# Kernel optimization log

Measured on AMD Instinct MI355X. Metric: run time of the kernel, lower is better.

Reference implementation:

```python
import jax, jax.numpy as jnp
import numpy as np

T, D, FF, E, R = 4096, 1024, 2048, 4, 16
LORA_SCALE = 32.0 / 16.0  # alpha / r


def setup_inputs() -> dict:
    key = jax.random.key(0)
    ks = jax.random.split(key, 12)
    return {
        "x": jax.random.normal(ks[0], (T, D), jnp.float32),
        "gate_w": jax.random.normal(ks[1], (E, D), jnp.float32) * 0.03,
        "gate_up_w": jax.random.normal(ks[2], (D, 2 * FF), jnp.float32)[None].repeat(E, 0) * 0.0
                     + jax.random.normal(ks[2], (E, D, 2 * FF), jnp.float32) * 0.03,
        "gate_up_b": jax.random.normal(ks[3], (E, 2 * FF), jnp.float32) * 0.01,
        "down_w": jax.random.normal(ks[4], (E, FF, D), jnp.float32) * 0.02,
        "down_b": jax.random.normal(ks[5], (E, D), jnp.float32) * 0.01,
        "A_gate": jax.random.normal(ks[6], (E, R, D), jnp.float32) * 0.02,
        "B_gate": jax.random.normal(ks[7], (E, FF, R), jnp.float32) * 0.02,
        "A_up": jax.random.normal(ks[8], (E, R, D), jnp.float32) * 0.02,
        "B_up": jax.random.normal(ks[9], (E, FF, R), jnp.float32) * 0.02,
        "A_down": jax.random.normal(ks[10], (E, R, FF), jnp.float32) * 0.02,
        "B_down": jax.random.normal(ks[11], (E, D, R), jnp.float32) * 0.02,
        "top_k": 2,
    }


def reference(x, gate_w, gate_up_w, gate_up_b, down_w, down_b,
              A_gate, B_gate, A_up, B_up, A_down, B_down, top_k):
    t, d = x.shape
    e = gate_w.shape[0]
    # --- router: logits, softmax (fp32), top-k, renormalize ---
    router_logits = x @ gate_w.T                                   # [T,E]
    rw = jax.nn.softmax(router_logits.astype(jnp.float32), axis=1)
    top_w, sel = jax.lax.top_k(rw, top_k)                          # [T,k]
    top_w = top_w / jnp.sum(top_w, axis=-1, keepdims=True)
    top_w = top_w.astype(x.dtype)
    # dense per-token per-expert combine weights (scatter of top-k weights)
    w = jnp.zeros((t, e), x.dtype).at[jnp.arange(t)[:, None], sel].add(top_w)  # [T,E]
    # --- per-expert SwiGLU MLP with LoRA (vectorized over experts) ---
    gu = jnp.einsum('td,edf->etf', x, gate_up_w) + gate_up_b[:, None, :]       # [E,T,2FF]
    ff = gu.shape[-1] // 2
    gate = gu[..., :ff] + jnp.einsum('td,erd,efr->etf', x, A_gate, B_gate) * LORA_SCALE
    up = gu[..., ff:] + jnp.einsum('td,erd,efr->etf', x, A_up, B_up) * LORA_SCALE
    act = jax.nn.silu(gate) * up                                               # [E,T,FF]
    down = jnp.einsum('etf,efd->etd', act, down_w) + down_b[:, None, :]
    down = down + jnp.einsum('etf,erf,edr->etd', act, A_down, B_down) * LORA_SCALE
    # --- weighted scatter-combine ---
    final = jnp.einsum('etd,te->td', down, w)                                  # [T,D]
    return final, router_logits
```

## Files before the change

kernel.cpp:

```cpp
#include <hip/hip_runtime.h>

#define T_TOK 4096
#define DIM   1024
#define FFD   2048
#define NEXP  4
#define NRP   8704
#define MTILES 68

typedef unsigned short u16;
typedef __attribute__((ext_vector_type(8))) short short8;
typedef __attribute__((ext_vector_type(4))) float f32x4;
typedef __attribute__((ext_vector_type(8))) unsigned short u16x8;
typedef __attribute__((ext_vector_type(4))) unsigned short u16x4;

typedef __attribute__((address_space(1))) unsigned int as1_u32;
typedef __attribute__((address_space(3))) unsigned int as3_u32;

__device__ __forceinline__ u16 f2bf(float f) {
  union { float f; unsigned u; } v; v.f = f;
  unsigned u = v.u;
  return (u16)((u + 0x7fffu + ((u >> 16) & 1u)) >> 16);
}
__device__ __forceinline__ float bf2f(u16 h) {
  union { unsigned u; float f; } v; v.u = ((unsigned)h) << 16;
  return v.f;
}
__device__ __forceinline__ void gload16(const void* g, void* l) {
  __builtin_amdgcn_global_load_lds((const as1_u32*)g, (as3_u32*)l, 16, 0, 0);
}

__global__ void router_k(const float* __restrict__ x, const float* __restrict__ gw,
                         float* __restrict__ logits_out, int* __restrict__ sel,
                         float* __restrict__ selw) {
  int t = blockIdx.x;
  int lane = threadIdx.x;
  float xv[16];
#pragma unroll
  for (int i = 0; i < 16; ++i) xv[i] = x[(size_t)t * DIM + lane + i * 64];
  float l[4];
#pragma unroll
  for (int e = 0; e < 4; ++e) {
    float s = 0.f;
#pragma unroll
    for (int i = 0; i < 16; ++i) s += xv[i] * gw[e * DIM + lane + i * 64];
#pragma unroll
    for (int off = 32; off > 0; off >>= 1) s += __shfl_xor(s, off, 64);
    l[e] = s;
  }
  if (lane == 0) {
#pragma unroll
    for (int e = 0; e < 4; ++e) logits_out[(size_t)t * 4 + e] = l[e];
    int e0 = 0; float b0 = l[0];
    for (int e = 1; e < 4; ++e) if (l[e] > b0) { b0 = l[e]; e0 = e; }
    int e1 = -1; float b1 = -3.4e38f;
    for (int e = 0; e < 4; ++e) if (e != e0 && l[e] > b1) { b1 = l[e]; e1 = e; }
    float p1 = expf(b1 - b0);
    float w0 = 1.f / (1.f + p1);
    sel[2 * t] = e0; sel[2 * t + 1] = e1;
    selw[2 * t] = w0; selw[2 * t + 1] = 1.f - w0;
  }
}

__global__ void scan_k(const int* __restrict__ sel, int* __restrict__ pos,
                       int* __restrict__ offs, int* __restrict__ rowtok,
                       int* __restrict__ pairrow) {
  __shared__ int base[4];
  __shared__ int wsum[16];
  __shared__ int off_s[5];
  int tid = threadIdx.x, lane = tid & 63, wid = tid >> 6;
  if (tid < 4) base[tid] = 0;
  __syncthreads();
  for (int chunk = 0; chunk < 4; ++chunk) {
    int t = chunk * 1024 + tid;
    int e0 = sel[2 * t], e1 = sel[2 * t + 1];
    for (int e = 0; e < 4; ++e) {
      bool f = (e0 == e) || (e1 == e);
      unsigned long long m = __ballot(f);
      int within = __popcll(m & ((1ull << lane) - 1ull));
      if (lane == 0) wsum[wid] = __popcll(m);
      __syncthreads();
      int wbase = 0, tot = 0;
      for (int i = 0; i < 16; ++i) { int v = wsum[i]; if (i < wid) wbase += v; tot += v; }
      if (f) {
        int p = base[e] + wbase + within;
        if (e0 == e) pos[2 * t] = p; else pos[2 * t + 1] = p;
      }
      __syncthreads();
      if (tid == 0) base[e] += tot;
      __syncthreads();
    }
  }
  if (tid == 0) {
    int o = 0;
    for (int e = 0; e < 4; ++e) { off_s[e] = o; o += ((base[e] + 127) >> 7) << 7; }
    off_s[4] = o;
    for (int i = 0; i < 5; ++i) offs[i] = off_s[i];
  }
  __syncthreads();
  for (int r = tid; r < NRP; r += 1024) rowtok[r] = -1;
  __syncthreads();
  for (int t = tid; t < T_TOK; t += 1024) {
#pragma unroll
    for (int s = 0; s < 2; ++s) {
      int e = sel[2 * t + s];
      int rr = off_s[e] + pos[2 * t + s];
      pairrow[2 * t + s] = rr;
      rowtok[rr] = t;
    }
  }
}

__global__ void gather_k(const float* __restrict__ x, const int* __restrict__ rowtok,
                         u16* __restrict__ xg) {
  int r = blockIdx.x, tid = threadIdx.x;
  int t = rowtok[r];
  float4 v = make_float4(0.f, 0.f, 0.f, 0.f);
  if (t >= 0) v = ((const float4*)(x + (size_t)t * DIM))[tid];
  u16x4 o;
  o[0] = f2bf(v.x); o[1] = f2bf(v.y); o[2] = f2bf(v.z); o[3] = f2bf(v.w);
  ((u16x4*)(xg + (size_t)r * DIM))[tid] = o;
}

__global__ void cvtA_k(const float* __restrict__ Ag, const float* __restrict__ Au,
                       const float* __restrict__ Ad, u16* __restrict__ abgu,
                       u16* __restrict__ adb) {
  int g = blockIdx.x * 256 + threadIdx.x;
  if (g < 32768) {
    int flat = g * 4;
    int e = flat >> 15;
    int rem = flat & 32767;
    int q = rem >> 10;
    int d = rem & 1023;
    const float* src = (q < 16) ? (Ag + ((size_t)e * 16 + q) * DIM + d)
                                : (Au + ((size_t)e * 16 + (q - 16)) * DIM + d);
    float4 v = *(const float4*)src;
    u16x4 o; o[0] = f2bf(v.x); o[1] = f2bf(v.y); o[2] = f2bf(v.z); o[3] = f2bf(v.w);
    *(u16x4*)(abgu + (size_t)flat) = o;
  } else {
    int flat = (g - 32768) * 4;
    float4 v = *(const float4*)(Ad + flat);
    u16x4 o; o[0] = f2bf(v.x); o[1] = f2bf(v.y); o[2] = f2bf(v.z); o[3] = f2bf(v.w);
    *(u16x4*)(adb + (size_t)flat) = o;
  }
}

__global__ void xa_k(const u16* __restrict__ xg, const u16* __restrict__ abgu,
                     const int* __restrict__ offs, float* __restrict__ xagu) {
  int r0 = blockIdx.x * 2, lane = threadIdx.x;
  int e = 0;
  if (r0 >= offs[1]) e = 1;
  if (r0 >= offs[2]) e = 2;
  if (r0 >= offs[3]) e = 3;
  float x0[16], x1[16];
#pragma unroll
  for (int i = 0; i < 4; ++i) {
    u16x4 v0 = ((const u16x4*)(xg + (size_t)r0 * DIM))[lane + i * 64];
    u16x4 v1 = ((const u16x4*)(xg + (size_t)(r0 + 1) * DIM))[lane + i * 64];
#pragma unroll
    for (int j = 0; j < 4; ++j) { x0[i * 4 + j] = bf2f(v0[j]); x1[i * 4 + j] = bf2f(v1[j]); }
  }
  const u16* A = abgu + (size_t)e * 32 * DIM;
  for (int q = 0; q < 32; ++q) {
    float s0 = 0.f, s1 = 0.f;
#pragma unroll
    for (int i = 0; i < 4; ++i) {
      u16x4 av = ((const u16x4*)(A + (size_t)q * DIM))[lane + i * 64];
#pragma unroll
      for (int j = 0; j < 4; ++j) {
        float a = bf2f(av[j]);
        s0 += x0[i * 4 + j] * a; s1 += x1[i * 4 + j] * a;
      }
    }
#pragma unroll
    for (int off = 32; off > 0; off >>= 1) { s0 += __shfl_xor(s0, off, 64); s1 += __shfl_xor(s1, off, 64); }
    if (lane == 0) { xagu[(size_t)r0 * 32 + q] = s0; xagu[(size_t)(r0 + 1) * 32 + q] = s1; }
  }
}

__global__ void aad_k(const u16* __restrict__ act, const u16* __restrict__ adb,
                      const int* __restrict__ offs, float* __restrict__ aad) {
  int r0 = blockIdx.x * 2, lane = threadIdx.x;
  int e = 0;
  if (r0 >= offs[1]) e = 1;
  if (r0 >= offs[2]) e = 2;
  if (r0 >= offs[3]) e = 3;
  float x0[32], x1[32];
#pragma unroll
  for (int i = 0; i < 8; ++i) {
    u16x4 v0 = ((const u16x4*)(act + (size_t)r0 * FFD))[lane + i * 64];
    u16x4 v1 = ((const u16x4*)(act + (size_t)(r0 + 1) * FFD))[lane + i * 64];
#pragma unroll
    for (int j = 0; j < 4; ++j) { x0[i * 4 + j] = bf2f(v0[j]); x1[i * 4 + j] = bf2f(v1[j]); }
  }
  const u16* A = adb + (size_t)e * 16 * FFD;
  for (int q = 0; q < 16; ++q) {
    float s0 = 0.f, s1 = 0.f;
#pragma unroll
    for (int i = 0; i < 8; ++i) {
      u16x4 av = ((const u16x4*)(A + (size_t)q * FFD))[lane + i * 64];
#pragma unroll
      for (int j = 0; j < 4; ++j) {
        float a = bf2f(av[j]);
        s0 += x0[i * 4 + j] * a; s1 += x1[i * 4 + j] * a;
      }
    }
#pragma unroll
    for (int off = 32; off > 0; off >>= 1) { s0 += __shfl_xor(s0, off, 64); s1 += __shfl_xor(s1, off, 64); }
    if (lane == 0) { aad[(size_t)r0 * 16 + q] = s0; aad[(size_t)(r0 + 1) * 16 + q] = s1; }
  }
}

__global__ void transpose_k(const float* __restrict__ in, u16* __restrict__ out,
                            int K, int N) {
  int e = blockIdx.z;
  int n0 = blockIdx.x * 32, k0 = blockIdx.y * 32;
  const float* I = in + (size_t)e * K * N;
  u16* O = out + (size_t)e * N * K;
  __shared__ u16 tile[32][33];
#pragma unroll
  for (int i = 0; i < 4; ++i) {
    int k = k0 + threadIdx.y + i * 8;
    tile[threadIdx.y + i * 8][threadIdx.x] = f2bf(I[(size_t)k * N + n0 + threadIdx.x]);
  }
  __syncthreads();
#pragma unroll
  for (int i = 0; i < 4; ++i) {
    int n = n0 + threadIdx.y + i * 8;
    O[(size_t)n * K + k0 + threadIdx.x] = tile[threadIdx.x][threadIdx.y + i * 8];
  }
}

__global__ __launch_bounds__(256) void gemm1_k(
    const u16* __restrict__ xg, const u16* __restrict__ wgu_t,
    const float* __restrict__ gub, const float* __restrict__ Bg,
    const float* __restrict__ Bu, const float* __restrict__ xagu,
    const int* __restrict__ offs, u16* __restrict__ act) {
  __shared__ __align__(16) u16 sAB[8192];
  u16* sA = sAB;
  u16* sB = sAB + 4096;
  int tid = threadIdx.x, w = tid >> 6, lane = tid & 63;
  int orig = blockIdx.x;
  int wg = (orig & 7) * 272 + (orig >> 3);
  int f0 = (wg & 31) * 64;
  int row0 = (wg >> 5) * 128;
  int e = 0;
  if (row0 >= offs[1]) e = 1;
  if (row0 >= offs[2]) e = 2;
  if (row0 >= offs[3]) e = 3;

  int srow = w * 32 + (lane >> 2);
  int scol = ((lane & 3) ^ ((lane >> 3) & 3)) * 8;
  const u16* gA = xg + (size_t)(row0 + srow) * DIM + scol;
  int n1 = srow, n2 = srow + 16;
  int gr1 = (n1 < 64) ? (f0 + n1) : (2048 + f0 + n1 - 64);
  int gr2 = (n2 < 64) ? (f0 + n2) : (2048 + f0 + n2 - 64);
  const u16* gB1 = wgu_t + ((size_t)e << 22) + (size_t)gr1 * DIM + scol;
  const u16* gB2 = wgu_t + ((size_t)e << 22) + (size_t)gr2 * DIM + scol;
  u16* lA = sA + w * 1024;
  u16* lB = sB + w * 1024;
  int fo = (((lane >> 4) ^ ((lane >> 1) & 3))) * 8;

  f32x4 acc[2][8];
#pragma unroll
  for (int i = 0; i < 2; ++i)
#pragma unroll
    for (int j = 0; j < 8; ++j) acc[i][j] = f32x4{0.f, 0.f, 0.f, 0.f};

  for (int kk = 0; kk < DIM; kk += 32) {
    __syncthreads();
    gload16(gA + kk, lA);
    gload16(gA + 16 * DIM + kk, lA + 512);
    gload16(gB1 + kk, lB);
    gload16(gB2 + kk, lB + 512);
    __syncthreads();
    short8 a[2], b[8];
#pragma unroll
    for (int mi = 0; mi < 2; ++mi)
      a[mi] = *(const short8*)&sA[(w * 32 + mi * 16 + (lane & 15)) * 32 + fo];
#pragma unroll
    for (int ni = 0; ni < 8; ++ni)
      b[ni] = *(const short8*)&sB[(ni * 16 + (lane & 15)) * 32 + fo];
#pragma unroll
    for (int mi = 0; mi < 2; ++mi)
#pragma unroll
      for (int ni = 0; ni < 8; ++ni)
        acc[mi][ni] = __builtin_amdgcn_mfma_f32_16x16x32_bf16(a[mi], b[ni], acc[mi][ni], 0, 0, 0);
  }

  __syncthreads();
  {
    int r = tid >> 1, kh = tid & 1;
    int sw = (r >> 1) & 3;
    int o0 = r * 32 + ((2 * kh + 0) ^ sw) * 8;
    int o1 = r * 32 + ((2 * kh + 1) ^ sw) * 8;
    u16 tmp[16];
    if (kh == 0) {
#pragma unroll
      for (int q = 0; q < 16; ++q) tmp[q] = f2bf(2.f * xagu[(size_t)(row0 + r) * 32 + q]);
    } else {
#pragma unroll
      for (int q = 0; q < 16; ++q) tmp[q] = 0;
      tmp[0] = 0x3f80;
    }
    *(u16x8*)&sA[o0] = *(u16x8*)&tmp[0];
    *(u16x8*)&sA[o1] = *(u16x8*)&tmp[8];
    int f = (r < 64) ? (f0 + r) : (f0 + r - 64);
    const float* Bsrc = (r < 64) ? Bg : Bu;
    float bias = gub[e * 4096 + ((r < 64) ? f : (2048 + f))];
    if (kh == 0) {
#pragma unroll
      for (int q = 0; q < 16; ++q) tmp[q] = f2bf(Bsrc[((size_t)e * FFD + f) * 16 + q]);
    } else {
#pragma unroll
      for (int q = 0; q < 16; ++q) tmp[q] = 0;
      tmp[0] = f2bf(bias);
    }
    *(u16x8*)&sB[o0] = *(u16x8*)&tmp[0];
    *(u16x8*)&sB[o1] = *(u16x8*)&tmp[8];
  }
  __syncthreads();
  {
    short8 a[2], b[4];
#pragma unroll
    for (int mi = 0; mi < 2; ++mi)
      a[mi] = *(const short8*)&sA[(w * 32 + mi * 16 + (lane & 15)) * 32 + fo];
#pragma unroll
    for (int ni = 0; ni < 4; ++ni)
      b[ni] = *(const short8*)&sB[(ni * 16 + (lane & 15)) * 32 + fo];
#pragma unroll
    for (int mi = 0; mi < 2; ++mi)
#pragma unroll
      for (int ni = 0; ni < 4; ++ni)
        acc[mi][ni] = __builtin_amdgcn_mfma_f32_16x16x32_bf16(a[mi], b[ni], acc[mi][ni], 0, 0, 0);
  }
  __syncthreads();
  {
    int r = tid >> 1, kh = tid & 1;
    int sw = (r >> 1) & 3;
    int o0 = r * 32 + ((2 * kh + 0) ^ sw) * 8;
    int o1 = r * 32 + ((2 * kh + 1) ^ sw) * 8;
    u16 tmp[16];
    if (kh == 0) {
#pragma unroll
      for (int q = 0; q < 16; ++q) tmp[q] = f2bf(2.f * xagu[(size_t)(row0 + r) * 32 + 16 + q]);
    } else {
#pragma unroll
      for (int q = 0; q < 16; ++q) tmp[q] = 0;
      tmp[0] = 0x3f80;
    }
    *(u16x8*)&sA[o0] = *(u16x8*)&tmp[0];
    *(u16x8*)&sA[o1] = *(u16x8*)&tmp[8];
  }
  __syncthreads();
  {
    short8 a[2], b[4];
#pragma unroll
    for (int mi = 0; mi < 2; ++mi)
      a[mi] = *(const short8*)&sA[(w * 32 + mi * 16 + (lane & 15)) * 32 + fo];
#pragma unroll
    for (int ni = 0; ni < 4; ++ni)
      b[ni] = *(const short8*)&sB[((ni + 4) * 16 + (lane & 15)) * 32 + fo];
#pragma unroll
    for (int mi = 0; mi < 2; ++mi)
#pragma unroll
      for (int ni = 0; ni < 4; ++ni)
        acc[mi][ni + 4] = __builtin_amdgcn_mfma_f32_16x16x32_bf16(a[mi], b[ni], acc[mi][ni + 4], 0, 0, 0);
  }
  __syncthreads();
#pragma unroll
  for (int mi = 0; mi < 2; ++mi)
#pragma unroll
    for (int ni = 0; ni < 4; ++ni)
#pragma unroll
      for (int j = 0; j < 4; ++j) {
        int lr = w * 32 + mi * 16 + (lane >> 4) * 4 + j;
        int lc = ni * 16 + (lane & 15);
        float g = acc[mi][ni][j];
        float u = acc[mi][ni + 4][j];
        float s = g / (1.f + __expf(-g));
        sAB[lr * 64 + lc] = f2bf(s * u);
      }
  __syncthreads();
#pragma unroll
  for (int it = 0; it < 4; ++it) {
    int idx = it * 256 + tid;
    int rr = idx >> 3, c8 = (idx & 7) * 8;
    *(u16x8*)(act + (size_t)(row0 + rr) * FFD + f0 + c8) = *(const u16x8*)&sAB[rr * 64 + c8];
  }
}

__global__ __launch_bounds__(256) void gemm2_k(
    const u16* __restrict__ act, const u16* __restrict__ wd_t,
    const float* __restrict__ db, const float* __restrict__ Bd,
    const float* __restrict__ aad, const int* __restrict__ offs,
    u16* __restrict__ down) {
  __shared__ __align__(16) u16 sAB[8192];
  u16* sA = sAB;
  u16* sB = sAB + 4096;
  int tid = threadIdx.x, w = tid >> 6, lane = tid & 63;
  int orig = blockIdx.x;
  int wg = (orig & 7) * 68 + (orig >> 3);
  int n0 = (wg & 7) * 128;
  int row0 = (wg >> 3) * 128;
  int ks = blockIdx.y;
  size_t kbase = (size_t)ks * 1024;
  int e = 0;
  if (row0 >= offs[1]) e = 1;
  if (row0 >= offs[2]) e = 2;
  if (row0 >= offs[3]) e = 3;
  int wm = w >> 1, wn = w & 1;

  int srow = w * 32 + (lane >> 2);
  int scol = ((lane & 3) ^ ((lane >> 3) & 3)) * 8;
  const u16* gA = act + (size_t)(row0 + srow) * FFD + kbase + scol;
  const u16* gB = wd_t + (size_t)e * DIM * FFD + (size_t)(n0 + srow) * FFD + kbase + scol;
  u16* lA = sA + w * 1024;
  u16* lB = sB + w * 1024;
  int fo = (((lane >> 4) ^ ((lane >> 1) & 3))) * 8;

  f32x4 acc[4][4];
#pragma unroll
  for (int i = 0; i < 4; ++i)
#pragma unroll
    for (int j = 0; j < 4; ++j) acc[i][j] = f32x4{0.f, 0.f, 0.f, 0.f};

  for (int kk = 0; kk < 1024; kk += 32) {
    __syncthreads();
    gload16(gA + kk, lA);
    gload16(gA + 16 * FFD + kk, lA + 512);
    gload16(gB + kk, lB);
    gload16(gB + 16 * FFD + kk, lB + 512);
    __syncthreads();
    short8 a[4], b[4];
#pragma unroll
    for (int mi = 0; mi < 4; ++mi)
      a[mi] = *(const short8*)&sA[(wm * 64 + mi * 16 + (lane & 15)) * 32 + fo];
#pragma unroll
    for (int ni = 0; ni < 4; ++ni)
      b[ni] = *(const short8*)&sB[(wn * 64 + ni * 16 + (lane & 15)) * 32 + fo];
#pragma unroll
    for (int mi = 0; mi < 4; ++mi)
#pragma unroll
      for (int ni = 0; ni < 4; ++ni)
        acc[mi][ni] = __builtin_amdgcn_mfma_f32_16x16x32_bf16(a[mi], b[ni], acc[mi][ni], 0, 0, 0);
  }

  if (ks == 0) {
    __syncthreads();
    {
      int r = tid >> 1, kh = tid & 1;
      int sw = (r >> 1) & 3;
      int o0 = r * 32 + ((2 * kh + 0) ^ sw) * 8;
      int o1 = r * 32 + ((2 * kh + 1) ^ sw) * 8;
      u16 tmp[16];
      if (kh == 0) {
#pragma unroll
        for (int q = 0; q < 16; ++q) tmp[q] = f2bf(2.f * aad[(size_t)(row0 + r) * 16 + q]);
      } else {
#pragma unroll
        for (int q = 0; q < 16; ++q) tmp[q] = 0;
        tmp[0] = 0x3f80;
      }
      *(u16x8*)&sA[o0] = *(u16x8*)&tmp[0];
      *(u16x8*)&sA[o1] = *(u16x8*)&tmp[8];
      if (kh == 0) {
#pragma unroll
        for (int q = 0; q < 16; ++q) tmp[q] = f2bf(Bd[((size_t)e * DIM + n0 + r) * 16 + q]);
      } else {
#pragma unroll
        for (int q = 0; q < 16; ++q) tmp[q] = 0;
        tmp[0] = f2bf(db[e * DIM + n0 + r]);
      }
      *(u16x8*)&sB[o0] = *(u16x8*)&tmp[0];
      *(u16x8*)&sB[o1] = *(u16x8*)&tmp[8];
    }
    __syncthreads();
    {
      short8 a[4], b[4];
#pragma unroll
      for (int mi = 0; mi < 4; ++mi)
        a[mi] = *(const short8*)&sA[(wm * 64 + mi * 16 + (lane & 15)) * 32 + fo];
#pragma unroll
      for (int ni = 0; ni < 4; ++ni)
        b[ni] = *(const short8*)&sB[(wn * 64 + ni * 16 + (lane & 15)) * 32 + fo];
#pragma unroll
      for (int mi = 0; mi < 4; ++mi)
#pragma unroll
        for (int ni = 0; ni < 4; ++ni)
          acc[mi][ni] = __builtin_amdgcn_mfma_f32_16x16x32_bf16(a[mi], b[ni], acc[mi][ni], 0, 0, 0);
    }
  }
#pragma unroll
  for (int mi = 0; mi < 4; ++mi)
#pragma unroll
    for (int ni = 0; ni < 4; ++ni)
#pragma unroll
      for (int j = 0; j < 4; ++j) {
        int lr = wm * 64 + mi * 16 + (lane >> 4) * 4 + j;
        int lc = wn * 64 + ni * 16 + (lane & 15);
        down[((size_t)ks * NRP + row0 + lr) * DIM + n0 + lc] = f2bf(acc[mi][ni][j]);
      }
}

__global__ void combine_k(const u16* __restrict__ down, const int* __restrict__ pairrow,
                          const float* __restrict__ selw, float* __restrict__ out) {
  int t = blockIdx.x, tid = threadIdx.x;
  int r0 = pairrow[2 * t], r1 = pairrow[2 * t + 1];
  float w0 = selw[2 * t], w1 = selw[2 * t + 1];
  u16x4 a0 = *(const u16x4*)(down + ((size_t)r0) * DIM + tid * 4);
  u16x4 a1 = *(const u16x4*)(down + ((size_t)NRP + r0) * DIM + tid * 4);
  u16x4 b0 = *(const u16x4*)(down + ((size_t)r1) * DIM + tid * 4);
  u16x4 b1 = *(const u16x4*)(down + ((size_t)NRP + r1) * DIM + tid * 4);
  f32x4 o;
#pragma unroll
  for (int j = 0; j < 4; ++j)
    o[j] = w0 * (bf2f(a0[j]) + bf2f(a1[j])) + w1 * (bf2f(b0[j]) + bf2f(b1[j]));
  *(f32x4*)(out + (size_t)t * DIM + tid * 4) = o;
}

extern "C" void kernel_launch(void* const* d_in, const int* in_sizes, int n_in,
                              void* d_out, int out_size, void* d_ws, size_t ws_size,
                              hipStream_t stream) {
  const float* x         = (const float*)d_in[0];
  const float* gate_w    = (const float*)d_in[1];
  const float* gate_up_w = (const float*)d_in[2];
  const float* gate_up_b = (const float*)d_in[3];
  const float* down_w    = (const float*)d_in[4];
  const float* down_b    = (const float*)d_in[5];
  const float* A_gate    = (const float*)d_in[6];
  const float* B_gate    = (const float*)d_in[7];
  const float* A_up      = (const float*)d_in[8];
  const float* B_up      = (const float*)d_in[9];
  const float* A_down    = (const float*)d_in[10];
  const float* B_down    = (const float*)d_in[11];

  float* out_final  = (float*)d_out;
  float* out_logits = out_final + (size_t)T_TOK * DIM;

  char* ws = (char*)d_ws;
  size_t o = 0;
  auto take = [&](size_t bytes) -> void* {
    void* p = ws + o;
    o = (o + bytes + 255) & ~(size_t)255;
    return p;
  };
  int*   offs    = (int*)take(64);
  int*   sel     = (int*)take((size_t)T_TOK * 2 * 4);
  float* selw    = (float*)take((size_t)T_TOK * 2 * 4);
  int*   pos     = (int*)take((size_t)T_TOK * 2 * 4);
  int*   pairrow = (int*)take((size_t)T_TOK * 2 * 4);
  int*   rowtok  = (int*)take((size_t)NRP * 4);
  float* xagu    = (float*)take((size_t)NRP * 32 * 4);
  float* aadb    = (float*)take((size_t)NRP * 16 * 4);
  u16*   abgu    = (u16*)take((size_t)NEXP * 32 * DIM * 2);
  u16*   adb     = (u16*)take((size_t)NEXP * 16 * FFD * 2);
  u16*   xg      = (u16*)take((size_t)NRP * DIM * 2);
  u16*   actb    = (u16*)take((size_t)NRP * FFD * 2);
  u16*   downb   = (u16*)take((size_t)2 * NRP * DIM * 2);
  u16*   wgu_t   = (u16*)take((size_t)NEXP * 2 * FFD * DIM * 2);
  u16*   wd_t    = (u16*)take((size_t)NEXP * DIM * FFD * 2);
  (void)ws_size; (void)in_sizes; (void)n_in; (void)out_size;

  transpose_k<<<dim3(128, 32, NEXP), dim3(32, 8), 0, stream>>>(gate_up_w, wgu_t, DIM, 2 * FFD);
  transpose_k<<<dim3(32, 64, NEXP), dim3(32, 8), 0, stream>>>(down_w, wd_t, FFD, DIM);
  cvtA_k<<<256, 256, 0, stream>>>(A_gate, A_up, A_down, abgu, adb);

  router_k<<<T_TOK, 64, 0, stream>>>(x, gate_w, out_logits, sel, selw);
  scan_k<<<1, 1024, 0, stream>>>(sel, pos, offs, rowtok, pairrow);
  gather_k<<<NRP, 256, 0, stream>>>(x, rowtok, xg);
  xa_k<<<NRP / 2, 64, 0, stream>>>(xg, abgu, offs, xagu);
  gemm1_k<<<2176, 256, 0, stream>>>(xg, wgu_t, gate_up_b, B_gate, B_up, xagu, offs, actb);
  aad_k<<<NRP / 2, 64, 0, stream>>>(actb, adb, offs, aadb);
  gemm2_k<<<dim3(544, 2), 256, 0, stream>>>(actb, wd_t, down_b, B_down, aadb, offs, downb);
  combine_k<<<T_TOK, 256, 0, stream>>>(downb, pairrow, selw, out_final);
}
```

Before: 302.9 us.

## Double-buffer LDS in both expert GEMMs and drop XCD block swizzle

Both grouped GEMM kernels now use two LDS stages, so the global-to-LDS loads for the next K slice are issued before the MFMAs on the current slice, with one barrier per iteration instead of two. LDS per block doubles to 32 KB. The launch grids also change from a 1D grid with an XCD-aware block remap to plain 2D/3D grids indexed directly, which changes how tiles are spread across chiplets and how L2 reuse behaves. The larger LDS footprint may reduce the number of resident blocks per CU.

```diff
diff --git a/kernel.cpp b/kernel.cpp
--- a/kernel.cpp
+++ b/kernel.cpp
@@ -235,14 +235,10 @@
     const float* __restrict__ gub, const float* __restrict__ Bg,
     const float* __restrict__ Bu, const float* __restrict__ xagu,
     const int* __restrict__ offs, u16* __restrict__ act) {
-  __shared__ __align__(16) u16 sAB[8192];
-  u16* sA = sAB;
-  u16* sB = sAB + 4096;
+  __shared__ __align__(16) u16 sAB[16384];
   int tid = threadIdx.x, w = tid >> 6, lane = tid & 63;
-  int orig = blockIdx.x;
-  int wg = (orig & 7) * 272 + (orig >> 3);
-  int f0 = (wg & 31) * 64;
-  int row0 = (wg >> 5) * 128;
+  int f0 = blockIdx.x * 64;
+  int row0 = blockIdx.y * 128;
   int e = 0;
   if (row0 >= offs[1]) e = 1;
   if (row0 >= offs[2]) e = 2;
@@ -256,9 +252,8 @@
   int gr2 = (n2 < 64) ? (f0 + n2) : (2048 + f0 + n2 - 64);
   const u16* gB1 = wgu_t + ((size_t)e << 22) + (size_t)gr1 * DIM + scol;
   const u16* gB2 = wgu_t + ((size_t)e << 22) + (size_t)gr2 * DIM + scol;
-  u16* lA = sA + w * 1024;
-  u16* lB = sB + w * 1024;
   int fo = (((lane >> 4) ^ ((lane >> 1) & 3))) * 8;
+  int ar = (w * 32 + (lane & 15)) * 32 + fo;
 
   f32x4 acc[2][8];
 #pragma unroll
@@ -266,27 +261,59 @@
 #pragma unroll
     for (int j = 0; j < 8; ++j) acc[i][j] = f32x4{0.f, 0.f, 0.f, 0.f};
 
-  for (int kk = 0; kk < DIM; kk += 32) {
+  {
+    u16* dA = sAB + w * 1024;
+    u16* dB = sAB + 4096 + w * 1024;
+    gload16(gA, dA); gload16(gA + 16 * DIM, dA + 512);
+    gload16(gB1, dB); gload16(gB2, dB + 512);
+  }
+  __syncthreads();
+  for (int t = 0; t < 31; ++t) {
+    int b = t & 1;
+    {
+      int kk = (t + 1) * 32;
+      u16* dA = sAB + (1 - b) * 8192 + w * 1024;
+      u16* dB = sAB + (1 - b) * 8192 + 4096 + w * 1024;
+      gload16(gA + kk, dA); gload16(gA + 16 * DIM + kk, dA + 512);
+      gload16(gB1 + kk, dB); gload16(gB2 + kk, dB + 512);
+    }
+    {
+      const u16* cA = sAB + b * 8192;
+      const u16* cB = sAB + b * 8192 + 4096;
+      short8 a[2], bb[8];
+#pragma unroll
+      for (int mi = 0; mi < 2; ++mi)
+        a[mi] = *(const short8*)&cA[ar + mi * 512];
+#pragma unroll
+      for (int ni = 0; ni < 8; ++ni)
+        bb[ni] = *(const short8*)&cB[(ni * 16 + (lane & 15)) * 32 + fo];
+#pragma unroll
+      for (int mi = 0; mi < 2; ++mi)
+#pragma unroll
+        for (int ni = 0; ni < 8; ++ni)
+          acc[mi][ni] = __builtin_amdgcn_mfma_f32_16x16x32_bf16(a[mi], bb[ni], acc[mi][ni], 0, 0, 0);
+    }
     __syncthreads();
-    gload16(gA + kk, lA);
-    gload16(gA + 16 * DIM + kk, lA + 512);
-    gload16(gB1 + kk, lB);
-    gload16(gB2 + kk, lB + 512);
-    __syncthreads();
-    short8 a[2], b[8];
+  }
+  {
+    const u16* cA = sAB + 8192;
+    const u16* cB = sAB + 8192 + 4096;
+    short8 a[2], bb[8];
 #pragma unroll
     for (int mi = 0; mi < 2; ++mi)
-      a[mi] = *(const short8*)&sA[(w * 32 + mi * 16 + (lane & 15)) * 32 + fo];
+      a[mi] = *(const short8*)&cA[ar + mi * 512];
 #pragma unroll
     for (int ni = 0; ni < 8; ++ni)
-      b[ni] = *(const short8*)&sB[(ni * 16 + (lane & 15)) * 32 + fo];
+      bb[ni] = *(const short8*)&cB[(ni * 16 + (lane & 15)) * 32 + fo];
 #pragma unroll
     for (int mi = 0; mi < 2; ++mi)
 #pragma unroll
       for (int ni = 0; ni < 8; ++ni)
-        acc[mi][ni] = __builtin_amdgcn_mfma_f32_16x16x32_bf16(a[mi], b[ni], acc[mi][ni], 0, 0, 0);
-  }
-
+        acc[mi][ni] = __builtin_amdgcn_mfma_f32_16x16x32_bf16(a[mi], bb[ni], acc[mi][ni], 0, 0, 0);
+  }
+
+  u16* sA = sAB;
+  u16* sB = sAB + 4096;
   __syncthreads();
   {
     int r = tid >> 1, kh = tid & 1;
@@ -323,7 +350,7 @@
     short8 a[2], b[4];
 #pragma unroll
     for (int mi = 0; mi < 2; ++mi)
-      a[mi] = *(const short8*)&sA[(w * 32 + mi * 16 + (lane & 15)) * 32 + fo];
+      a[mi] = *(const short8*)&sA[ar + mi * 512];
 #pragma unroll
     for (int ni = 0; ni < 4; ++ni)
       b[ni] = *(const short8*)&sB[(ni * 16 + (lane & 15)) * 32 + fo];
@@ -356,7 +383,7 @@
     short8 a[2], b[4];
 #pragma unroll
     for (int mi = 0; mi < 2; ++mi)
-      a[mi] = *(const short8*)&sA[(w * 32 + mi * 16 + (lane & 15)) * 32 + fo];
+      a[mi] = *(const short8*)&sA[ar + mi * 512];
 #pragma unroll
     for (int ni = 0; ni < 4; ++ni)
       b[ni] = *(const short8*)&sB[((ni + 4) * 16 + (lane & 15)) * 32 + fo];
@@ -394,15 +421,11 @@
     const float* __restrict__ db, const float* __restrict__ Bd,
     const float* __restrict__ aad, const int* __restrict__ offs,
     u16* __restrict__ down) {
-  __shared__ __align__(16) u16 sAB[8192];
-  u16* sA = sAB;
-  u16* sB = sAB + 4096;
+  __shared__ __align__(16) u16 sAB[16384];
   int tid = threadIdx.x, w = tid >> 6, lane = tid & 63;
-  int orig = blockIdx.x;
-  int wg = (orig & 7) * 68 + (orig >> 3);
-  int n0 = (wg & 7) * 128;
-  int row0 = (wg >> 3) * 128;
-  int ks = blockIdx.y;
+  int n0 = blockIdx.x * 128;
+  int row0 = blockIdx.y * 128;
+  int ks = blockIdx.z;
   size_t kbase = (size_t)ks * 1024;
   int e = 0;
   if (row0 >= offs[1]) e = 1;
@@ -414,9 +437,9 @@
   int scol = ((lane & 3) ^ ((lane >> 3) & 3)) * 8;
   const u16* gA = act + (size_t)(row0 + srow) * FFD + kbase + scol;
   const u16* gB = wd_t + (size_t)e * DIM * FFD + (size_t)(n0 + srow) * FFD + kbase + scol;
-  u16* lA = sA + w * 1024;
-  u16* lB = sB + w * 1024;
   int fo = (((lane >> 4) ^ ((lane >> 1) & 3))) * 8;
+  int ar = (wm * 64 + (lane & 15)) * 32 + fo;
+  int br = (wn * 64 + (lane & 15)) * 32 + fo;
 
   f32x4 acc[4][4];
 #pragma unroll
@@ -424,27 +447,59 @@
 #pragma unroll
     for (int j = 0; j < 4; ++j) acc[i][j] = f32x4{0.f, 0.f, 0.f, 0.f};
 
-  for (int kk = 0; kk < 1024; kk += 32) {
+  {
+    u16* dA = sAB + w * 1024;
+    u16* dB = sAB + 4096 + w * 1024;
+    gload16(gA, dA); gload16(gA + 16 * FFD, dA + 512);
+    gload16(gB, dB); gload16(gB + 16 * FFD, dB + 512);
+  }
+  __syncthreads();
+  for (int t = 0; t < 31; ++t) {
+    int b = t & 1;
+    {
+      int kk = (t + 1) * 32;
+      u16* dA = sAB + (1 - b) * 8192 + w * 1024;
+      u16* dB = sAB + (1 - b) * 8192 + 4096 + w * 1024;
+      gload16(gA + kk, dA); gload16(gA + 16 * FFD + kk, dA + 512);
+      gload16(gB + kk, dB); gload16(gB + 16 * FFD + kk, dB + 512);
+    }
+    {
+      const u16* cA = sAB + b * 8192;
+      const u16* cB = sAB + b * 8192 + 4096;
+      short8 a[4], bb[4];
+#pragma unroll
+      for (int mi = 0; mi < 4; ++mi)
+        a[mi] = *(const short8*)&cA[ar + mi * 512];
+#pragma unroll
+      for (int ni = 0; ni < 4; ++ni)
+        bb[ni] = *(const short8*)&cB[br + ni * 512];
+#pragma unroll
+      for (int mi = 0; mi < 4; ++mi)
+#pragma unroll
+        for (int ni = 0; ni < 4; ++ni)
+          acc[mi][ni] = __builtin_amdgcn_mfma_f32_16x16x32_bf16(a[mi], bb[ni], acc[mi][ni], 0, 0, 0);
+    }
     __syncthreads();
-    gload16(gA + kk, lA);
-    gload16(gA + 16 * FFD + kk, lA + 512);
-    gload16(gB + kk, lB);
-    gload16(gB + 16 * FFD + kk, lB + 512);
-    __syncthreads();
-    short8 a[4], b[4];
+  }
+  {
+    const u16* cA = sAB + 8192;
+    const u16* cB = sAB + 8192 + 4096;
+    short8 a[4], bb[4];
 #pragma unroll
     for (int mi = 0; mi < 4; ++mi)
-      a[mi] = *(const short8*)&sA[(wm * 64 + mi * 16 + (lane & 15)) * 32 + fo];
+      a[mi] = *(const short8*)&cA[ar + mi * 512];
 #pragma unroll
     for (int ni = 0; ni < 4; ++ni)
-      b[ni] = *(const short8*)&sB[(wn * 64 + ni * 16 + (lane & 15)) * 32 + fo];
+      bb[ni] = *(const short8*)&cB[br + ni * 512];
 #pragma unroll
     for (int mi = 0; mi < 4; ++mi)
 #pragma unroll
       for (int ni = 0; ni < 4; ++ni)
-        acc[mi][ni] = __builtin_amdgcn_mfma_f32_16x16x32_bf16(a[mi], b[ni], acc[mi][ni], 0, 0, 0);
-  }
-
+        acc[mi][ni] = __builtin_amdgcn_mfma_f32_16x16x32_bf16(a[mi], bb[ni], acc[mi][ni], 0, 0, 0);
+  }
+
+  u16* sA = sAB;
+  u16* sB = sAB + 4096;
   if (ks == 0) {
     __syncthreads();
     {
@@ -479,10 +534,10 @@
       short8 a[4], b[4];
 #pragma unroll
       for (int mi = 0; mi < 4; ++mi)
-        a[mi] = *(const short8*)&sA[(wm * 64 + mi * 16 + (lane & 15)) * 32 + fo];
+        a[mi] = *(const short8*)&sA[ar + mi * 512];
 #pragma unroll
       for (int ni = 0; ni < 4; ++ni)
-        b[ni] = *(const short8*)&sB[(wn * 64 + ni * 16 + (lane & 15)) * 32 + fo];
+        b[ni] = *(const short8*)&sB[br + ni * 512];
 #pragma unroll
       for (int mi = 0; mi < 4; ++mi)
 #pragma unroll
@@ -569,8 +624,9 @@
   scan_k<<<1, 1024, 0, stream>>>(sel, pos, offs, rowtok, pairrow);
   gather_k<<<NRP, 256, 0, stream>>>(x, rowtok, xg);
   xa_k<<<NRP / 2, 64, 0, stream>>>(xg, abgu, offs, xagu);
-  gemm1_k<<<2176, 256, 0, stream>>>(xg, wgu_t, gate_up_b, B_gate, B_up, xagu, offs, actb);
+  gemm1_k<<<dim3(32, MTILES), 256, 0, stream>>>(xg, wgu_t, gate_up_b, B_gate, B_up,
+                                                xagu, offs, actb);
   aad_k<<<NRP / 2, 64, 0, stream>>>(actb, adb, offs, aadb);
-  gemm2_k<<<dim3(544, 2), 256, 0, stream>>>(actb, wd_t, down_b, B_down, aadb, offs, downb);
+  gemm2_k<<<dim3(8, MTILES, 2), 256, 0, stream>>>(actb, wd_t, down_b, B_down, aadb, offs, downb);
   combine_k<<<T_TOK, 256, 0, stream>>>(downb, pairrow, selw, out_final);
 }
```

Result: faster. 289.7 us (-4.3%).
